# Kernel optimization log

Hardware: AMD Instinct MI355X
Metric: run time of the kernel (lower is better)

## Reference

```python
import jax, jax.numpy as jnp
import numpy as np

# Model dims (match init_kwargs)
B, S, D = 4, 2048, 1024          # batch, seq, d_model
H, E, DH = 8, 4, 128             # n_heads, n_experts_attn, d_head
K = 2                            # k_attn (routed, n_expert_shared_attn=0)
NEG_INF = jnp.float32(-1e30)


def setup_inputs() -> dict:
    key = jax.random.key(0)
    ks = jax.random.split(key, 9)
    s = np.float32(1.0 / np.sqrt(D))
    return {
        "q_src": jax.random.normal(ks[0], (B, S, D), jnp.float32),
        "k_src": jax.random.normal(ks[1], (B, S, D), jnp.float32),
        "v_src": jax.random.normal(ks[2], (B, S, D), jnp.float32),
        "wq": jax.random.normal(ks[3], (H * DH, D), jnp.float32) * s,
        "wk": jax.random.normal(ks[4], (H * DH, D), jnp.float32) * s,
        "sel_v_w": jax.random.normal(ks[5], (H * E, D), jnp.float32) * s,
        "sel_o_w": jax.random.normal(ks[6], (H * E, D), jnp.float32) * s,
        "v_w": jax.random.normal(ks[7], (H, E, D, DH), jnp.float32) * s,
        "o_w": jax.random.normal(ks[8], (H, E, DH, D), jnp.float32) * np.float32(1.0 / np.sqrt(H * DH)),
        "bias_v": jnp.zeros((E,), jnp.float32),   # load-balancing bias buffer (zeros at init)
        "bias_o": jnp.zeros((E,), jnp.float32),
        # causal boolean mask, True = attend (skip_mask all True -> trimming is identity)
        "attn_mask": jnp.broadcast_to(jnp.tril(jnp.ones((S, S), bool)), (B, S, S)),
        "position_ids": jnp.broadcast_to(jnp.arange(S, dtype=jnp.int32), (B, S)),
        "skip_mask": jnp.ones((B, S), bool),
    }


def _expert_gate(x, w, bias):
    """Sigmoid gating + per-head top-k routed expert selection.
    Returns dense combine weights [b,s,h,E] (sum of sel_val * one_hot) and indices [b,s,h,K]."""
    logits = (x @ w.T).reshape(*x.shape[:-1], H, E)        # [b,s,h,E]
    sel = jax.nn.sigmoid(logits)
    # bias only affects *which* experts are picked (added under no_grad in torch)
    _, idx = jax.lax.top_k(jax.lax.stop_gradient(sel) + bias, K)  # [b,s,h,K]
    sel_val = jnp.take_along_axis(sel, idx, axis=-1)        # [b,s,h,K]
    gate = jnp.sum(jax.nn.one_hot(idx, E, dtype=sel.dtype) * sel_val[..., None], axis=-2)
    return gate, idx


def reference(q_src, k_src, v_src, wq, wk, sel_v_w, sel_o_w, v_w, o_w,
              bias_v, bias_o, attn_mask, position_ids, skip_mask):
    # scale.sqrt() applied to both q and k -> full 1/sqrt(d_head) on scores
    ssq = jnp.float32((1.0 / np.sqrt(DH)) ** 0.5)
    q = ((q_src @ wq.T) * ssq).reshape(B, S, H, DH).transpose(0, 2, 1, 3)  # [b,h,s,dh]
    k = ((k_src @ wk.T) * ssq).reshape(B, S, H, DH).transpose(0, 2, 1, 3)

    v_gate, v_idx = _expert_gate(k_src, sel_v_w, bias_v)    # V experts routed on k_src
    o_gate, o_idx = _expert_gate(q_src, sel_o_w, bias_o)    # O experts routed on q_src

    # expert-mixed V projection (cvmm): all experts then dense combine
    all_v = jnp.einsum('bsm,hemd->bshed', v_src, v_w)       # [b,s,h,E,dh]
    v = jnp.einsum('bshed,bshe->bhsd', all_v, v_gate)       # [b,h,s,dh]

    scores = jnp.einsum('bhqd,bhkd->bhqk', q, k)
    scores = jnp.where(attn_mask[:, None], scores, NEG_INF)
    attn = jax.nn.softmax(scores, axis=-1)
    out = jnp.einsum('bhqk,bhkd->bqhd', attn, v)            # [b,s,h,dh]

    # expert-mixed O projection, summed over heads
    scaled = out[..., None, :] * o_gate[..., None]          # [b,s,h,E,dh]
    res = jnp.einsum('bshed,hedm->bsm', scaled, o_w)        # [b,s,d_model]
    return res, (v_idx, o_idx)
```

## Files before the change

### kernel.cpp

```cpp
#include <hip/hip_runtime.h>
#include <cstdint>
#include <cstddef>

typedef __bf16 bf16;
typedef __bf16 bf16x4 __attribute__((ext_vector_type(4)));
typedef __bf16 bf16x8 __attribute__((ext_vector_type(8)));
typedef float  fx4    __attribute__((ext_vector_type(4)));


__device__ __forceinline__ void async16(const bf16* g, bf16* l) {
  __builtin_amdgcn_global_load_lds((const __attribute__((address_space(1))) void*)g,
                                   (__attribute__((address_space(3))) void*)l, 16, 0, 0);
}

#define BARRIER() do { asm volatile("" ::: "memory"); __builtin_amdgcn_s_barrier(); \
                       asm volatile("" ::: "memory"); } while (0)

template <int CTRL>
__device__ __forceinline__ float dppf(float x) {
  return __int_as_float(__builtin_amdgcn_update_dpp(
      0, __float_as_int(x), CTRL, 0xf, 0xf, true));
}

__global__ __launch_bounds__(256) void f32_to_bf16(const float4* __restrict__ src,
                                                   bf16x4* __restrict__ dst, int n4) {
  int i = blockIdx.x * 256 + threadIdx.x;
  if (i < n4) {
    float4 v = src[i];
    bf16x4 o;
    o[0] = (bf16)v.x; o[1] = (bf16)v.y; o[2] = (bf16)v.z; o[3] = (bf16)v.w;
    dst[i] = o;
  }
}

__global__ __launch_bounds__(256) void make_wvt(const float* __restrict__ v_w,
                                                bf16* __restrict__ wvt) {
  __shared__ float tile[64][65];
  const int he = blockIdx.z, k0 = blockIdx.x * 64, dh0 = blockIdx.y * 64;
  const float* in = v_w + (size_t)he * 1024 * 128;
  #pragma unroll
  for (int j = 0; j < 16; j++) {
    int idx = threadIdx.x + j * 256;
    int r = idx >> 6, c = idx & 63;
    tile[r][c] = in[(size_t)(k0 + r) * 128 + dh0 + c];
  }
  __syncthreads();
  const int h = he >> 2, e = he & 3;
  bf16* outp = wvt + ((size_t)(h * 128 + dh0) * 4 + e) * 1024 + k0;
  #pragma unroll
  for (int j = 0; j < 16; j++) {
    int idx = threadIdx.x + j * 256;
    int r = idx >> 6, c = idx & 63;
    outp[(size_t)r * 4096 + c] = (bf16)tile[c][r];
  }
}

__global__ __launch_bounds__(256) void make_wot(const float* __restrict__ o_w,
                                                bf16* __restrict__ wot) {
  __shared__ float tile[64][65];
  const int he = blockIdx.z, d0 = blockIdx.x * 64, dh0 = blockIdx.y * 64;
  const float* in = o_w + (size_t)he * 128 * 1024;
  #pragma unroll
  for (int j = 0; j < 16; j++) {
    int idx = threadIdx.x + j * 256;
    int r = idx >> 6, c = idx & 63;
    tile[r][c] = in[(size_t)(dh0 + r) * 1024 + d0 + c];
  }
  __syncthreads();
  bf16* outp = wot + (size_t)d0 * 4096 + he * 128 + dh0;
  #pragma unroll
  for (int j = 0; j < 16; j++) {
    int idx = threadIdx.x + j * 256;
    int r = idx >> 6, c = idx & 63;
    outp[(size_t)r * 4096 + c] = (bf16)tile[c][r];
  }
}

__global__ __launch_bounds__(256) void gating(const float* __restrict__ q_src,
                                              const float* __restrict__ k_src,
                                              const float* __restrict__ sel_v_w,
                                              const float* __restrict__ sel_o_w,
                                              const float* __restrict__ bias_v,
                                              const float* __restrict__ bias_o,
                                              float* __restrict__ gate_v,
                                              float* __restrict__ gate_o,
                                              float* __restrict__ d_out) {
  int m = blockIdx.x, g = blockIdx.y;
  const float* x = g ? q_src : k_src;
  const float* w = g ? sel_o_w : sel_v_w;
  const float* bias = g ? bias_o : bias_v;
  float* gate = g ? gate_o : gate_v;
  float* idxo = d_out + 8388608 + g * 131072;

  __shared__ float xs[1024];
  __shared__ double part_s[32][8];
  __shared__ double sel_s[32];
  int t = threadIdx.x;
  #pragma unroll
  for (int p = 0; p < 4; p++) xs[t + p * 256] = x[(size_t)m * 1024 + t + p * 256];
  __syncthreads();
  int he = t >> 3, pp = t & 7;
  const float* wrow = w + he * 1024;
  double acc = 0.0;
  for (int j = 0; j < 128; j++) { int k = pp + j * 8; acc += (double)xs[k] * (double)wrow[k]; }
  part_s[he][pp] = acc;
  __syncthreads();
  if (t < 32) {
    double tot = 0.0;
    #pragma unroll
    for (int j = 0; j < 8; j++) tot += part_s[t][j];
    sel_s[t] = 1.0 / (1.0 + exp(-tot));
  }
  __syncthreads();
  if (t < 8) {
    double v[4], vbv[4];
    #pragma unroll
    for (int e = 0; e < 4; e++) { v[e] = sel_s[t * 4 + e]; vbv[e] = v[e] + (double)bias[e]; }
    int i0 = 0;
    for (int e = 1; e < 4; e++) if (vbv[e] > vbv[i0]) i0 = e;
    int i1 = -1; double best = -1e300;
    for (int e = 0; e < 4; e++) { if (e == i0) continue; if (vbv[e] > best) { best = vbv[e]; i1 = e; } }
    float* gp = gate + ((size_t)m * 8 + t) * 4;
    #pragma unroll
    for (int e = 0; e < 4; e++) {
      float gv = 0.f;
      if (e == i0) gv = (float)v[i0];
      else if (e == i1) gv = (float)v[i1];
      gp[e] = gv;
    }
    idxo[m * 16 + t * 2 + 0] = (float)i0;
    idxo[m * 16 + t * 2 + 1] = (float)i1;
  }
}

__global__ __launch_bounds__(256) void expand_o(const bf16* __restrict__ outb,
                                                const float* __restrict__ gate_o,
                                                bf16* __restrict__ Ae) {
  int idx = blockIdx.x * 256 + threadIdx.x;
  int m = idx >> 9;
  int u = idx & 511;
  int he = u >> 4;
  int hh = he >> 2, e = he & 3;
  int dh0 = (u & 15) * 8;
  float gv = gate_o[((size_t)m * 8 + hh) * 4 + e];
  bf16x8 v = *(const bf16x8*)(outb + ((size_t)m * 8 + hh) * 128 + dh0);
  #pragma unroll
  for (int j = 0; j < 8; j++) v[j] = (bf16)((float)v[j] * gv);
  *(bf16x8*)(Ae + (size_t)m * 4096 + u * 8) = v;
}

template <int MODE>
__global__ __launch_bounds__(512) void gemm_moe(const bf16* __restrict__ Abf,
                                                const bf16* __restrict__ BT,
                                                const float* __restrict__ gate,
                                                bf16* __restrict__ Cbf,
                                                float* __restrict__ Cf32,
                                                float scale) {
  constexpr int KDIM = (MODE == 0) ? 1024 : 4096;
  constexpr int ASTRIDE = (MODE == 2) ? 4096 : 1024;
  __shared__ __align__(16) bf16 smem[49152];
  const int t = threadIdx.x;
  const int wave = t >> 6, lane = t & 63;
  const int wr = wave >> 1, wc = wave & 1;
  const int quad = lane >> 4, l16 = lane & 15;
  const int bid = blockIdx.x;
  const int m0 = (bid >> 3) * 256;
  const int n0 = (MODE == 1) ? 0 : (bid & 7) * 128;
  const int h = (MODE == 1) ? (bid & 7) : 0;
  const bf16* BTh = (MODE == 1) ? BT + (size_t)h * 128 * 4096 : BT;

  fx4 acc[4][4] = {};
  fx4 accT[4][4] = {};

  const int srow = t >> 3, sch = t & 7;

  auto stage = [&](int buf, int k0) {
    bf16* As = smem + buf * 16384;
    bf16* Bs = smem + 32768 + buf * 8192;
    #pragma unroll
    for (int p = 0; p < 2; p++) {
      int row = p * 64 + srow;
      int sc = sch ^ (row & 7);
      async16(BTh + (size_t)(n0 + row) * KDIM + k0 + sc * 8,
              Bs + row * 64 + sch * 8);
    }
    int col = (MODE == 1) ? (k0 & 1023) : k0;
    #pragma unroll
    for (int p = 0; p < 4; p++) {
      int row = p * 64 + srow;
      int sc = sch ^ (row & 7);
      async16(Abf + (size_t)(m0 + row) * ASTRIDE + col + sc * 8,
              As + row * 64 + sch * 8);
    }
  };

  stage(0, 0);
  int buf = 0;
  for (int k0 = 0; k0 < KDIM; k0 += 64) {
    if (k0 + 64 < KDIM) {
      stage(buf ^ 1, k0 + 64);
      asm volatile("s_waitcnt vmcnt(6)" ::: "memory");
    } else {
      asm volatile("s_waitcnt vmcnt(0)" ::: "memory");
    }
    BARRIER();
    const bf16* As = smem + buf * 16384;
    const bf16* Bs = smem + 32768 + buf * 8192;
    #pragma unroll
    for (int kk = 0; kk < 64; kk += 32) {
      bf16x8 af[4], bfr[4];
      #pragma unroll
      for (int i = 0; i < 4; i++) {
        int ar = wr * 64 + i * 16 + l16;
        af[i] = *(const bf16x8*)(As + ar * 64 + ((((kk >> 3) + quad) ^ (ar & 7)) * 8));
      }
      #pragma unroll
      for (int i = 0; i < 2; i++) {
        int br = wc * 64 + i * 16 + l16;
        bfr[i] = *(const bf16x8*)(Bs + br * 64 + ((((kk >> 3) + quad) ^ (br & 7)) * 8));
      }
      BARRIER();
      __builtin_amdgcn_s_setprio(1);
      #pragma unroll
      for (int mi = 0; mi < 4; mi++)
        #pragma unroll
        for (int ni = 0; ni < 2; ni++)
          acc[mi][ni] = __builtin_amdgcn_mfma_f32_16x16x32_bf16(af[mi], bfr[ni], acc[mi][ni], 0, 0, 0);
      __builtin_amdgcn_s_setprio(0);
      BARRIER();
      #pragma unroll
      for (int i = 2; i < 4; i++) {
        int br = wc * 64 + i * 16 + l16;
        bfr[i] = *(const bf16x8*)(Bs + br * 64 + ((((kk >> 3) + quad) ^ (br & 7)) * 8));
      }
      BARRIER();
      __builtin_amdgcn_s_setprio(1);
      #pragma unroll
      for (int mi = 0; mi < 4; mi++)
        #pragma unroll
        for (int ni = 2; ni < 4; ni++)
          acc[mi][ni] = __builtin_amdgcn_mfma_f32_16x16x32_bf16(af[mi], bfr[ni], acc[mi][ni], 0, 0, 0);
      __builtin_amdgcn_s_setprio(0);
      BARRIER();
    }
    if constexpr (MODE == 1) {
      if (((k0 + 64) & 1023) == 0) {
        const int e = k0 >> 10;
        #pragma unroll
        for (int mi = 0; mi < 4; mi++)
          #pragma unroll
          for (int r = 0; r < 4; r++) {
            int m = m0 + wr * 64 + mi * 16 + quad * 4 + r;
            float gv = gate[((size_t)m * 8 + h) * 4 + e];
            #pragma unroll
            for (int ni = 0; ni < 4; ni++)
              accT[mi][ni][r] += gv * acc[mi][ni][r];
          }
        #pragma unroll
        for (int mi = 0; mi < 4; mi++)
          #pragma unroll
          for (int ni = 0; ni < 4; ni++)
            #pragma unroll
            for (int j = 0; j < 4; j++) acc[mi][ni][j] = 0.f;
      }
    }
    buf ^= 1;
  }

  if (MODE == 1) {
    #pragma unroll
    for (int mi = 0; mi < 4; mi++)
      #pragma unroll
      for (int ni = 0; ni < 4; ni++) {
        int nl = wc * 64 + ni * 16 + l16;
        int ml = wr * 64 + mi * 16 + quad * 4;
        bf16x4 pk;
        #pragma unroll
        for (int r = 0; r < 4; r++) pk[r] = (bf16)accT[mi][ni][r];
        *(bf16x4*)(smem + nl * 264 + ml) = pk;
      }
    __syncthreads();
    int b = m0 >> 11, s0 = m0 & 2047;
    const int row = t >> 2, seg = t & 3;
    bf16* dst = Cbf + (((size_t)(b * 8 + h) * 128) + row) * 2048 + s0 + seg * 64;
    #pragma unroll
    for (int j = 0; j < 8; j++)
      *(float4*)(dst + j * 8) = *(float4*)(smem + row * 264 + seg * 64 + j * 8);
    return;
  }

  #pragma unroll
  for (int mi = 0; mi < 4; mi++)
    #pragma unroll
    for (int ni = 0; ni < 4; ni++)
      #pragma unroll
      for (int r = 0; r < 4; r++) {
        int m = m0 + wr * 64 + mi * 16 + quad * 4 + r;
        int n = n0 + wc * 64 + ni * 16 + l16;
        float v = acc[mi][ni][r] * scale;
        if (MODE == 0) {
          int b = m >> 11, s = m & 2047, hh = n >> 7, dh = n & 127;
          Cbf[(((size_t)(b * 8 + hh) * 2048 + s) << 7) + dh] = (bf16)v;
        } else {
          Cf32[(size_t)m * 1024 + n] = v;
        }
      }
}

__global__ __launch_bounds__(256) void attn_kernel(const bf16* __restrict__ qb,
                                                   const bf16* __restrict__ kb,
                                                   const bf16* __restrict__ vbT,
                                                   bf16* __restrict__ outb) {
  const int bh = blockIdx.y;
  const int b = bh >> 3, h = bh & 7;
  __shared__ __align__(16) bf16 Ks[2][64 * 128];
  __shared__ __align__(16) bf16 VTs[2][128 * 64];
  __shared__ __align__(16) bf16 Ps[4][16][72];
  const int t = threadIdx.x, wave = t >> 6, lane = t & 63;
  const int quad = lane >> 4, l16 = lane & 15;
  const bf16* qbase  = qb  + (size_t)bh * 2048 * 128;
  const bf16* kbase  = kb  + (size_t)bh * 2048 * 128;
  const bf16* vtbase = vbT + (size_t)bh * 128 * 2048;

  auto stage = [&](int buf, int kt) {
    #pragma unroll
    for (int p = 0; p < 4; p++) {
      int o = p * 4096 + wave * 1024 + lane * 16;
      int kr = o >> 8, kc = o & 255;
      async16((const bf16*)((const char*)kbase + (size_t)(kt * 64 + kr) * 256 + (kc ^ ((kr & 7) << 4))),
              (bf16*)((char*)&Ks[buf][0] + o));
    }
    #pragma unroll
    for (int p = 0; p < 4; p++) {
      int o = p * 4096 + wave * 1024 + lane * 16;
      int vr = o >> 7, vc = o & 127;
      async16((const bf16*)((const char*)vtbase + (size_t)vr * 4096 + kt * 128 + (vc ^ ((vr & 7) << 4))),
              (bf16*)((char*)&VTs[buf][0] + o));
    }
  };

  #pragma unroll 1
  for (int pass = 0; pass < 2; pass++) {
    const int qt = pass ? blockIdx.x : (31 - blockIdx.x);

    bf16x8 qf[4];
    #pragma unroll
    for (int dk = 0; dk < 4; dk++)
      qf[dk] = *(const bf16x8*)(qbase + (size_t)(qt * 64 + wave * 16 + l16) * 128 + dk * 32 + quad * 8);

    float m_run[4], l_run[4];
    fx4 acc_o[8] = {};
    #pragma unroll
    for (int r = 0; r < 4; r++) { m_run[r] = -1e30f; l_run[r] = 0.f; }

    stage(0, 0);
    int cur = 0;

    for (int kt = 0; kt <= qt; kt++) {
      if (kt < qt) {
        stage(cur ^ 1, kt + 1);
        asm volatile("s_waitcnt vmcnt(8)" ::: "memory");
      } else {
        asm volatile("s_waitcnt vmcnt(0)" ::: "memory");
      }
      __builtin_amdgcn_s_barrier();
      asm volatile("" ::: "memory");

      const char* Ksb  = (const char*)&Ks[cur][0];
      const char* VTsb = (const char*)&VTs[cur][0];

      fx4 accs[4] = {};
      __builtin_amdgcn_s_setprio(1);
      #pragma unroll
      for (int ni = 0; ni < 4; ni++)
        #pragma unroll
        for (int dk = 0; dk < 4; dk++) {
          int r = ni * 16 + l16;
          bf16x8 kf = *(const bf16x8*)(Ksb + r * 256 + ((dk * 64 + quad * 16) ^ ((r & 7) << 4)));
          accs[ni] = __builtin_amdgcn_mfma_f32_16x16x32_bf16(qf[dk], kf, accs[ni], 0, 0, 0);
        }
      __builtin_amdgcn_s_setprio(0);

      if (kt == qt) {
        #pragma unroll
        for (int ni = 0; ni < 4; ni++)
          #pragma unroll
          for (int r = 0; r < 4; r++) {
            int qr = wave * 16 + quad * 4 + r;
            int kc = ni * 16 + l16;
            if (kc > qr) accs[ni][r] = -1e30f;
          }
      }

      #pragma unroll
      for (int r = 0; r < 4; r++) {
        float mx = fmaxf(fmaxf(accs[0][r], accs[1][r]), fmaxf(accs[2][r], accs[3][r]));
        mx = fmaxf(mx, dppf<0x121>(mx));
        mx = fmaxf(mx, dppf<0x122>(mx));
        mx = fmaxf(mx, dppf<0x124>(mx));
        mx = fmaxf(mx, dppf<0x128>(mx));
        float m_new = fmaxf(m_run[r], mx);
        float alpha = __builtin_amdgcn_exp2f(m_run[r] - m_new);
        float rs = 0.f;
        #pragma unroll
        for (int ni = 0; ni < 4; ni++) {
          float p = __builtin_amdgcn_exp2f(accs[ni][r] - m_new);
          accs[ni][r] = p; rs += p;
        }
        rs += dppf<0x121>(rs);
        rs += dppf<0x122>(rs);
        rs += dppf<0x124>(rs);
        rs += dppf<0x128>(rs);
        l_run[r] = l_run[r] * alpha + rs;
        m_run[r] = m_new;
        #pragma unroll
        for (int nj = 0; nj < 8; nj++) acc_o[nj][r] *= alpha;
      }

      #pragma unroll
      for (int ni = 0; ni < 4; ni++)
        #pragma unroll
        for (int r = 0; r < 4; r++)
          Ps[wave][quad * 4 + r][ni * 16 + l16] = (bf16)accs[ni][r];

      __builtin_amdgcn_s_setprio(1);
      #pragma unroll
      for (int step = 0; step < 2; step++) {
        bf16x8 pf = *(const bf16x8*)&Ps[wave][l16][step * 32 + quad * 8];
        #pragma unroll
        for (int nj = 0; nj < 8; nj++) {
          int r = nj * 16 + l16;
          bf16x8 vf = *(const bf16x8*)(VTsb + r * 128 + ((step * 64 + quad * 16) ^ ((r & 7) << 4)));
          acc_o[nj] = __builtin_amdgcn_mfma_f32_16x16x32_bf16(pf, vf, acc_o[nj], 0, 0, 0);
        }
      }
      __builtin_amdgcn_s_setprio(0);

      asm volatile("" ::: "memory");
      __builtin_amdgcn_s_barrier();
      cur ^= 1;
    }

    #pragma unroll
    for (int nj = 0; nj < 8; nj++)
      #pragma unroll
      for (int r = 0; r < 4; r++) {
        int s = qt * 64 + wave * 16 + quad * 4 + r;
        int token = b * 2048 + s;
        float o = acc_o[nj][r] / l_run[r];
        outb[((size_t)token * 8 + h) * 128 + nj * 16 + l16] = (bf16)o;
      }
  }
}

extern "C" void kernel_launch(void* const* d_in, const int* in_sizes, int n_in,
                              void* d_out, int out_size, void* d_ws, size_t ws_size,
                              hipStream_t stream) {
  const float* q_src  = (const float*)d_in[0];
  const float* k_src  = (const float*)d_in[1];
  const float* v_src  = (const float*)d_in[2];
  const float* wq     = (const float*)d_in[3];
  const float* wk     = (const float*)d_in[4];
  const float* sel_v_w = (const float*)d_in[5];
  const float* sel_o_w = (const float*)d_in[6];
  const float* v_w    = (const float*)d_in[7];
  const float* o_w    = (const float*)d_in[8];
  const float* bias_v = (const float*)d_in[9];
  const float* bias_o = (const float*)d_in[10];
  float* out = (float*)d_out;

  char* ws = (char*)d_ws;
  size_t off = 0;
  auto alloc = [&](size_t bytes) { char* p = ws + off; off += (bytes + 255) & ~(size_t)255; return p; };
  bf16* wqb   = (bf16*)alloc((size_t)1024 * 1024 * 2);
  bf16* wkb   = (bf16*)alloc((size_t)1024 * 1024 * 2);
  bf16* wvt   = (bf16*)alloc((size_t)8 * 128 * 4 * 1024 * 2);
  bf16* wot   = (bf16*)alloc((size_t)1024 * 4096 * 2);
  float* gate_v = (float*)alloc((size_t)8192 * 32 * 4);
  float* gate_o = (float*)alloc((size_t)8192 * 32 * 4);
  bf16* qsb   = (bf16*)alloc((size_t)8192 * 1024 * 2);
  bf16* ksb   = (bf16*)alloc((size_t)8192 * 1024 * 2);
  bf16* vsb   = (bf16*)alloc((size_t)8192 * 1024 * 2);
  bf16* qb    = (bf16*)alloc((size_t)8192 * 1024 * 2);
  bf16* kb    = (bf16*)alloc((size_t)8192 * 1024 * 2);
  bf16* vbT   = (bf16*)alloc((size_t)8192 * 1024 * 2);
  bf16* outb  = (bf16*)alloc((size_t)8192 * 1024 * 2);
  bf16* Ae    = qsb;

  f32_to_bf16<<<1024, 256, 0, stream>>>((const float4*)wq, (bf16x4*)wqb, 262144);
  f32_to_bf16<<<1024, 256, 0, stream>>>((const float4*)wk, (bf16x4*)wkb, 262144);
  f32_to_bf16<<<8192, 256, 0, stream>>>((const float4*)q_src, (bf16x4*)qsb, 2097152);
  f32_to_bf16<<<8192, 256, 0, stream>>>((const float4*)k_src, (bf16x4*)ksb, 2097152);
  f32_to_bf16<<<8192, 256, 0, stream>>>((const float4*)v_src, (bf16x4*)vsb, 2097152);
  make_wvt<<<dim3(16, 2, 32), 256, 0, stream>>>(v_w, wvt);
  make_wot<<<dim3(16, 2, 32), 256, 0, stream>>>(o_w, wot);
  gating<<<dim3(8192, 2), 256, 0, stream>>>(q_src, k_src, sel_v_w, sel_o_w,
                                            bias_v, bias_o, gate_v, gate_o, out);

  const float ssq = 0.29730177875068026f;
  const float log2e = 1.4426950408889634f;
  gemm_moe<0><<<256, 512, 0, stream>>>(qsb, wqb, nullptr, qb, nullptr, ssq * log2e);
  gemm_moe<0><<<256, 512, 0, stream>>>(ksb, wkb, nullptr, kb, nullptr, ssq);
  gemm_moe<1><<<256, 512, 0, stream>>>(vsb, wvt, gate_v, vbT, nullptr, 1.0f);
  attn_kernel<<<dim3(16, 32), 256, 0, stream>>>(qb, kb, vbT, outb);
  expand_o<<<16384, 256, 0, stream>>>(outb, gate_o, Ae);
  gemm_moe<2><<<256, 512, 0, stream>>>(Ae, wot, nullptr, nullptr, out, 1.0f);
}
```

Measured before the change: 646.8 us.

## Tile gating kernel over 64 tokens with double-buffered async LDS staging

The gating kernel previously ran one block per token and reloaded the full 32x1024 selector weight matrix for each one. It now processes 64 tokens per block, streaming x and w chunks of 128 columns into swizzled, double-buffered LDS with async global-to-LDS loads. Each thread accumulates 2 tokens by 4 experts in double precision, and the sigmoid is now computed in float via exp2. The intent is to cut redundant weight traffic and the many tiny blocks. The cost is only 256 blocks and heavy fp64 FMA work per thread, and the float sigmoid may differ slightly near top-k ties.

```diff
diff --git a/kernel.cpp b/kernel.cpp
--- a/kernel.cpp
+++ b/kernel.cpp
@@ -8,7 +8,7 @@
 typedef float  fx4    __attribute__((ext_vector_type(4)));
 
 
-__device__ __forceinline__ void async16(const bf16* g, bf16* l) {
+__device__ __forceinline__ void async16(const void* g, void* l) {
   __builtin_amdgcn_global_load_lds((const __attribute__((address_space(1))) void*)g,
                                    (__attribute__((address_space(3))) void*)l, 16, 0, 0);
 }
@@ -85,51 +85,99 @@
                                               float* __restrict__ gate_v,
                                               float* __restrict__ gate_o,
                                               float* __restrict__ d_out) {
-  int m = blockIdx.x, g = blockIdx.y;
+  const int g = blockIdx.y;
+  const int m0 = blockIdx.x * 64;
   const float* x = g ? q_src : k_src;
   const float* w = g ? sel_o_w : sel_v_w;
   const float* bias = g ? bias_o : bias_v;
   float* gate = g ? gate_o : gate_v;
   float* idxo = d_out + 8388608 + g * 131072;
 
-  __shared__ float xs[1024];
-  __shared__ double part_s[32][8];
-  __shared__ double sel_s[32];
-  int t = threadIdx.x;
-  #pragma unroll
-  for (int p = 0; p < 4; p++) xs[t + p * 256] = x[(size_t)m * 1024 + t + p * 256];
-  __syncthreads();
-  int he = t >> 3, pp = t & 7;
-  const float* wrow = w + he * 1024;
-  double acc = 0.0;
-  for (int j = 0; j < 128; j++) { int k = pp + j * 8; acc += (double)xs[k] * (double)wrow[k]; }
-  part_s[he][pp] = acc;
-  __syncthreads();
-  if (t < 32) {
-    double tot = 0.0;
-    #pragma unroll
-    for (int j = 0; j < 8; j++) tot += part_s[t][j];
-    sel_s[t] = 1.0 / (1.0 + exp(-tot));
-  }
-  __syncthreads();
-  if (t < 8) {
-    double v[4], vbv[4];
-    #pragma unroll
-    for (int e = 0; e < 4; e++) { v[e] = sel_s[t * 4 + e]; vbv[e] = v[e] + (double)bias[e]; }
+  __shared__ __align__(16) float smem[2 * 12288];
+
+  const int t = threadIdx.x;
+  const int hg = t & 7;
+  const int tg = t >> 3;
+
+  auto stage = [&](int buf, int k0) {
+    float* xs = smem + buf * 12288;
+    float* ws = xs + 8192;
+    #pragma unroll
+    for (int p = 0; p < 8; p++) {
+      int of = p * 1024 + t * 4;
+      int row = of >> 7, c = (of >> 2) & 31;
+      int sc = c ^ ((row >> 1) & 7);
+      async16(x + (size_t)(m0 + row) * 1024 + k0 + sc * 4, xs + of);
+    }
+    #pragma unroll
+    for (int p = 0; p < 4; p++) {
+      int of = p * 1024 + t * 4;
+      int row = of >> 7, c = (of >> 2) & 31;
+      int sc = c ^ ((row >> 2) & 7);
+      async16(w + (size_t)row * 1024 + k0 + sc * 4, ws + of);
+    }
+  };
+
+  double acc[2][4] = {};
+
+  stage(0, 0);
+  int buf = 0;
+  for (int c8 = 0; c8 < 8; c8++) {
+    if (c8 < 7) {
+      stage(buf ^ 1, (c8 + 1) * 128);
+      asm volatile("s_waitcnt vmcnt(12)" ::: "memory");
+    } else {
+      asm volatile("s_waitcnt vmcnt(0)" ::: "memory");
+    }
+    BARRIER();
+    const float* xs = smem + buf * 12288;
+    const float* ws = xs + 8192;
+    const int xr0 = tg * 2;
+    #pragma unroll 4
+    for (int k4 = 0; k4 < 32; k4++) {
+      float4 x0 = *(const float4*)(xs + (size_t)xr0 * 128 + (size_t)((k4 ^ (tg & 7)) * 4));
+      float4 x1 = *(const float4*)(xs + (size_t)(xr0 + 1) * 128 + (size_t)((k4 ^ (tg & 7)) * 4));
+      double x0d[4] = {(double)x0.x, (double)x0.y, (double)x0.z, (double)x0.w};
+      double x1d[4] = {(double)x1.x, (double)x1.y, (double)x1.z, (double)x1.w};
+      #pragma unroll
+      for (int e = 0; e < 4; e++) {
+        int wr = hg * 4 + e;
+        float4 wv = *(const float4*)(ws + (size_t)wr * 128 + (size_t)((k4 ^ hg) * 4));
+        double w0 = (double)wv.x, w1 = (double)wv.y, w2 = (double)wv.z, w3 = (double)wv.w;
+        acc[0][e] += x0d[0] * w0 + x0d[1] * w1 + x0d[2] * w2 + x0d[3] * w3;
+        acc[1][e] += x1d[0] * w0 + x1d[1] * w1 + x1d[2] * w2 + x1d[3] * w3;
+      }
+    }
+    BARRIER();
+    buf ^= 1;
+  }
+
+  const float log2e = 1.4426950408889634f;
+  float b0 = bias[0], b1 = bias[1], b2 = bias[2], b3 = bias[3];
+  #pragma unroll
+  for (int tok = 0; tok < 2; tok++) {
+    int m = m0 + tg * 2 + tok;
+    float sel[4];
+    #pragma unroll
+    for (int e = 0; e < 4; e++) {
+      float lv = (float)acc[tok][e];
+      sel[e] = 1.0f / (1.0f + __builtin_amdgcn_exp2f(-lv * log2e));
+    }
+    float vb[4] = {sel[0] + b0, sel[1] + b1, sel[2] + b2, sel[3] + b3};
     int i0 = 0;
-    for (int e = 1; e < 4; e++) if (vbv[e] > vbv[i0]) i0 = e;
-    int i1 = -1; double best = -1e300;
-    for (int e = 0; e < 4; e++) { if (e == i0) continue; if (vbv[e] > best) { best = vbv[e]; i1 = e; } }
-    float* gp = gate + ((size_t)m * 8 + t) * 4;
-    #pragma unroll
-    for (int e = 0; e < 4; e++) {
-      float gv = 0.f;
-      if (e == i0) gv = (float)v[i0];
-      else if (e == i1) gv = (float)v[i1];
-      gp[e] = gv;
-    }
-    idxo[m * 16 + t * 2 + 0] = (float)i0;
-    idxo[m * 16 + t * 2 + 1] = (float)i1;
+    #pragma unroll
+    for (int e = 1; e < 4; e++) if (vb[e] > vb[i0]) i0 = e;
+    int i1 = -1; float best = -1e30f;
+    #pragma unroll
+    for (int e = 0; e < 4; e++) { if (e == i0) continue; if (vb[e] > best) { best = vb[e]; i1 = e; } }
+    float4 gv;
+    gv.x = (i0 == 0 || i1 == 0) ? sel[0] : 0.f;
+    gv.y = (i0 == 1 || i1 == 1) ? sel[1] : 0.f;
+    gv.z = (i0 == 2 || i1 == 2) ? sel[2] : 0.f;
+    gv.w = (i0 == 3 || i1 == 3) ? sel[3] : 0.f;
+    *(float4*)(gate + ((size_t)m * 8 + hg) * 4) = gv;
+    idxo[m * 16 + hg * 2 + 0] = (float)i0;
+    idxo[m * 16 + hg * 2 + 1] = (float)i1;
   }
 }
 
@@ -327,15 +375,15 @@
     for (int p = 0; p < 4; p++) {
       int o = p * 4096 + wave * 1024 + lane * 16;
       int kr = o >> 8, kc = o & 255;
-      async16((const bf16*)((const char*)kbase + (size_t)(kt * 64 + kr) * 256 + (kc ^ ((kr & 7) << 4))),
-              (bf16*)((char*)&Ks[buf][0] + o));
+      async16((const char*)kbase + (size_t)(kt * 64 + kr) * 256 + (kc ^ ((kr & 7) << 4)),
+              (char*)&Ks[buf][0] + o);
     }
     #pragma unroll
     for (int p = 0; p < 4; p++) {
       int o = p * 4096 + wave * 1024 + lane * 16;
       int vr = o >> 7, vc = o & 127;
-      async16((const bf16*)((const char*)vtbase + (size_t)vr * 4096 + kt * 128 + (vc ^ ((vr & 7) << 4))),
-              (bf16*)((char*)&VTs[buf][0] + o));
+      async16((const char*)vtbase + (size_t)vr * 4096 + kt * 128 + (vc ^ ((vr & 7) << 4)),
+              (char*)&VTs[buf][0] + o);
     }
   };
 
@@ -494,8 +542,8 @@
   f32_to_bf16<<<8192, 256, 0, stream>>>((const float4*)v_src, (bf16x4*)vsb, 2097152);
   make_wvt<<<dim3(16, 2, 32), 256, 0, stream>>>(v_w, wvt);
   make_wot<<<dim3(16, 2, 32), 256, 0, stream>>>(o_w, wot);
-  gating<<<dim3(8192, 2), 256, 0, stream>>>(q_src, k_src, sel_v_w, sel_o_w,
-                                            bias_v, bias_o, gate_v, gate_o, out);
+  gating<<<dim3(128, 2), 256, 0, stream>>>(q_src, k_src, sel_v_w, sel_o_w,
+                                           bias_v, bias_o, gate_v, gate_o, out);
 
   const float ssq = 0.29730177875068026f;
   const float log2e = 1.4426950408889634f;
```

Measured after the change: 597.4 us. 7.6% less time.
